# Kernel tuning notes

Measured on AMD Instinct MI355X. Metric: run time of the kernel, lower is better.

## Reference

```python
import jax, jax.numpy as jnp
import numpy as np


def squash(s, axis=-1):
    sq = jnp.sum(jnp.square(s), axis=axis, keepdims=True)
    scale = sq / (1.0 + sq) / (jnp.sqrt(sq) + 1e-08)
    return scale * s


def setup_inputs() -> dict:
    key = jax.random.key(0)
    k1, k2 = jax.random.split(key)
    # [B, input_num_caps, input_dim_caps]
    x = jax.random.normal(k1, (64, 1152, 8), dtype=jnp.float32)
    # W: [input_num_caps, num_capsules, input_dim_caps, dim_capsules]
    W = jax.random.normal(k2, (1152, 32, 8, 16), dtype=jnp.float32) * 0.05
    return {"x": x, "W": W}


def reference(x, W):
    # Original tiles x along the output-capsule axis before the einsum
    # 'bicd,icde->bice'; since the tiled copies are identical along c,
    # this is exactly 'bid,icde->bice' without materializing the tile.
    u_hat = jnp.einsum('bid,icde->bice', x, W)  # [B, I, C, E]
    b = jnp.zeros(u_hat.shape[:3], dtype=u_hat.dtype)  # [B, I, C]
    routings = 3
    v = None
    for i in range(routings):
        c = jax.nn.softmax(b, axis=-1)                 # over output capsules
        s = jnp.einsum('bic,bice->bce', c, u_hat)      # weighted sum over I
        v = squash(s)                                  # [B, C, E]
        if i < routings - 1:
            b = b + jnp.einsum('bice,bce->bic', u_hat, v)  # agreement
    return v
```

## Files before the change

### kernel.cpp

```cpp
#include <hip/hip_runtime.h>
#include <hip/hip_fp16.h>

#define B_ 64
#define I_ 1152
#define C_ 32
#define E_ 16
#define D_ 8
#define BC_ 8
#define ICt 12
#define NIC (I_/ICt)
#define ICX (NIC/8)
#define WROW4 (C_*D_*E_/4)
#define SCE (B_*C_*E_)
#define SCE2 (SCE/2)
#define WIB 8192

__device__ __forceinline__ void gload_lds16(const void* g, void* l) {
  typedef __attribute__((address_space(1))) const void GV;
  typedef __attribute__((address_space(3))) void LV;
  __builtin_amdgcn_global_load_lds((GV*)g, (LV*)l, 16, 0, 0);
}

#define WAITVM8() do { asm volatile("s_waitcnt vmcnt(8)" ::: "memory"); \
                       __builtin_amdgcn_sched_barrier(0); } while (0)
#define WAITVM4() do { asm volatile("s_waitcnt vmcnt(4)" ::: "memory"); \
                       __builtin_amdgcn_sched_barrier(0); } while (0)
#define WAITVM0() do { asm volatile("s_waitcnt vmcnt(0)" ::: "memory"); \
                       __builtin_amdgcn_sched_barrier(0); } while (0)
#define WAITLG0() do { asm volatile("s_waitcnt lgkmcnt(0)" ::: "memory"); \
                       __builtin_amdgcn_sched_barrier(0); } while (0)

typedef _Float16 h2v __attribute__((ext_vector_type(2)));

__device__ __forceinline__ float dot2f(__half2 a, __half2 b, float c) {
#if defined(__has_builtin)
#if __has_builtin(__builtin_amdgcn_fdot2)
  return __builtin_amdgcn_fdot2(__builtin_bit_cast(h2v, a),
                                __builtin_bit_cast(h2v, b), c, false);
#else
  float2 fa = __half22float2(a), fb = __half22float2(b);
  return fmaf(fa.x, fb.x, fmaf(fa.y, fb.y, c));
#endif
#else
  float2 fa = __half22float2(a), fb = __half22float2(b);
  return fmaf(fa.x, fb.x, fmaf(fa.y, fb.y, c));
#endif
}

__device__ __forceinline__ float h2bits(float a, float b) {
  return __builtin_bit_cast(float, __float22half2_rn({a, b}));
}

__global__ __launch_bounds__(256)
void caps_pass0(const float* __restrict__ x, const float* __restrict__ W,
                __half* __restrict__ partial, __half* __restrict__ Wh,
                __half2* __restrict__ xh)
{
  __shared__ float4 Wl[3][1024];
  __shared__ float4 xl[BC_*ICt*2];

  const int t     = threadIdx.x;
  const int c     = t & 31;
  const int eh    = (t >> 5) & 1;
  const int bq    = t >> 6;
  const int xcd   = blockIdx.x & 7;
  const int sl    = blockIdx.x >> 3;
  const int ic    = xcd * ICX + (sl >> 3);
  const int bslab = sl & 7;
  const int b0    = bslab * BC_;
  const int i0    = ic * ICt;

  int fsrc[4];
#pragma unroll
  for (int k = 0; k < 4; ++k) {
    int cc = (t >> 5) + 8*k;
    fsrc[k] = cc*32 + ((c - cc) & 31);
  }

  if (t < BC_*ICt*2) {
    int b = t / (ICt*2), r = t % (ICt*2);
    xl[t] = ((const float4*)x)[ ((size_t)(b0 + b)*I_ + i0)*2 + r ];
  }

  const float4* wg = (const float4*)(W + (size_t)i0 * (C_*D_*E_));
#pragma unroll
  for (int k = 0; k < 4; ++k) gload_lds16(wg + fsrc[k],          &Wl[0][t + 256*k]);
#pragma unroll
  for (int k = 0; k < 4; ++k) gload_lds16(wg + WROW4 + fsrc[k],  &Wl[1][t + 256*k]);

  float acc[2][8];
#pragma unroll
  for (int j = 0; j < 2; ++j)
#pragma unroll
    for (int e = 0; e < 8; ++e) acc[j][e] = 0.f;

  int cur = 0;
  for (int ii = 0; ii < ICt; ++ii) {
    WAITLG0();
    __builtin_amdgcn_s_barrier();
    __builtin_amdgcn_sched_barrier(0);

    if (ii + 2 < ICt) {
      int pre = cur + 2; if (pre >= 3) pre -= 3;
      const float4* wn = wg + (size_t)(ii + 2) * WROW4;
#pragma unroll
      for (int k = 0; k < 4; ++k)
        gload_lds16(wn + fsrc[k], &Wl[pre][t + 256*k]);
    }

    if (ii < ICt - 2)       WAITVM8();
    else if (ii == ICt - 2) WAITVM4();
    else                    WAITVM0();
    __builtin_amdgcn_s_barrier();
    __builtin_amdgcn_sched_barrier(0);

    __builtin_amdgcn_s_setprio(1);
    float xv[2][8];
#pragma unroll
    for (int j = 0; j < 2; ++j) {
      float4 a = xl[(bq*2 + j)*(ICt*2) + ii*2 + 0];
      float4 b = xl[(bq*2 + j)*(ICt*2) + ii*2 + 1];
      xv[j][0]=a.x; xv[j][1]=a.y; xv[j][2]=a.z; xv[j][3]=a.w;
      xv[j][4]=b.x; xv[j][5]=b.y; xv[j][6]=b.z; xv[j][7]=b.w;
    }

    float uh[2][8];
#pragma unroll
    for (int j = 0; j < 2; ++j)
#pragma unroll
      for (int e = 0; e < 8; ++e) uh[j][e] = 0.f;

#pragma unroll
    for (int d = 0; d < D_; ++d) {
#pragma unroll
      for (int qq = 0; qq < 2; ++qq) {
        float4 wv = Wl[cur][c*32 + (((d*4 + eh*2 + qq) + c) & 31)];
        const int eb = qq*4;
#pragma unroll
        for (int j = 0; j < 2; ++j) {
          uh[j][eb+0] = fmaf(xv[j][d], wv.x, uh[j][eb+0]);
          uh[j][eb+1] = fmaf(xv[j][d], wv.y, uh[j][eb+1]);
          uh[j][eb+2] = fmaf(xv[j][d], wv.z, uh[j][eb+2]);
          uh[j][eb+3] = fmaf(xv[j][d], wv.w, uh[j][eb+3]);
        }
      }
    }

#pragma unroll
    for (int j = 0; j < 2; ++j)
#pragma unroll
      for (int e = 0; e < 8; ++e) acc[j][e] = fmaf((1.0f/C_), uh[j][e], acc[j][e]);
    __builtin_amdgcn_s_setprio(0);

    cur = (cur + 1 == 3) ? 0 : cur + 1;
  }

#pragma unroll
  for (int j = 0; j < 2; ++j) {
    size_t base = ((size_t)ic * B_ + (b0 + bq*2 + j)) * (C_*E_) + (size_t)c*E_ + eh*8;
    float4 o;
    o.x = h2bits(acc[j][0], acc[j][1]);
    o.y = h2bits(acc[j][2], acc[j][3]);
    o.z = h2bits(acc[j][4], acc[j][5]);
    o.w = h2bits(acc[j][6], acc[j][7]);
    *(float4*)(partial + base) = o;
  }

  for (int ii = bslab; ii < ICt; ii += 8) {
    const int i = i0 + ii;
    const float4* src = (const float4*)(W + (size_t)i * (C_*D_*E_));
#pragma unroll
    for (int g = 0; g < 2; ++g) {
      int G  = t*2 + g;
      int cc = G >> 4, q = G & 15;
      int d  = q >> 1, eo = q & 1;
      const float4* s4 = src + (cc*8 + d)*4 + eo*2;
      float4 a = s4[0], b = s4[1];
      float4 o;
      o.x = h2bits(a.x, a.y); o.y = h2bits(a.z, a.w);
      o.z = h2bits(b.x, b.y); o.w = h2bits(b.z, b.w);
      *(float4*)(Wh + (size_t)i * 4096 + G*8) = o;
    }
  }
  if (t < BC_*ICt*2) {
    int b = t / (ICt*2), r = t % (ICt*2);
    float4 a = xl[t];
    float4 o;
    o.x = h2bits(a.x, a.x); o.y = h2bits(a.y, a.y);
    o.z = h2bits(a.z, a.z); o.w = h2bits(a.w, a.w);
    size_t idx = ((size_t)(b0 + b)*I_ + (i0 + (r >> 1)))*D_ + (r & 1)*4;
    *(float4*)(xh + idx) = o;
  }
}

template<int MODE>
__global__ __launch_bounds__(256)
void caps_pass_f16(const __half2* __restrict__ xh, const char* __restrict__ Wh,
                   const float* __restrict__ vacc, __half* __restrict__ partial)
{
  __shared__ float4 Wl[3][1024];
  __shared__ __half2 xl[BC_*ICt*D_];

  const int t   = threadIdx.x;
  const int c   = t & 31;
  const int eh  = (t >> 5) & 1;
  const int bq  = t >> 6;
  const int xcd = blockIdx.x & 7;
  const int sl  = blockIdx.x >> 3;
  const int ic  = xcd * ICX + (sl >> 3);
  const int b0  = (sl & 7) * BC_;
  const int i0  = ic * ICt;

  int fsrc[2];
#pragma unroll
  for (int k = 0; k < 2; ++k) {
    int g = t + 256*k, cc = g >> 4, q = g & 15;
    fsrc[k] = cc*256 + ((q ^ (cc & 15)) << 4);
  }

  __half2 vrp[2][4];
#pragma unroll
  for (int j = 0; j < 2; ++j) {
    const float4* vp = (const float4*)(vacc + (((size_t)(b0 + bq*2 + j)*C_ + c)*E_ + eh*8));
    float4 a = vp[0], b = vp[1];
    vrp[j][0] = __float22half2_rn({a.x, a.y});
    vrp[j][1] = __float22half2_rn({a.z, a.w});
    vrp[j][2] = __float22half2_rn({b.x, b.y});
    vrp[j][3] = __float22half2_rn({b.z, b.w});
  }

  if (t < BC_*ICt*D_/4) {
    int b = t / 24, r = t % 24;
    float4 v = ((const float4*)(xh + ((size_t)(b0 + b)*I_ + i0)*D_))[r];
    ((float4*)xl)[b*24 + r] = v;
  }

  const char* wg = Wh + (size_t)i0 * WIB;
#pragma unroll
  for (int k = 0; k < 4; ++k)
    gload_lds16(wg + (k>>1)*WIB + fsrc[k&1], (char*)&Wl[0][0] + (t + 256*k)*16);
#pragma unroll
  for (int k = 0; k < 4; ++k)
    gload_lds16(wg + WIB*2 + (k>>1)*WIB + fsrc[k&1], (char*)&Wl[1][0] + (t + 256*k)*16);

  __half2 accp[2][4];
#pragma unroll
  for (int j = 0; j < 2; ++j)
#pragma unroll
    for (int q = 0; q < 4; ++q) accp[j][q] = __half2{__half(0.f), __half(0.f)};

  int cur = 0;
  for (int p = 0; p < ICt/2; ++p) {
    WAITLG0();
    __builtin_amdgcn_s_barrier();
    __builtin_amdgcn_sched_barrier(0);

    if (p + 2 < ICt/2) {
      int pre = cur + 2; if (pre >= 3) pre -= 3;
      const char* wn = wg + (size_t)(p + 2) * (2*WIB);
#pragma unroll
      for (int k = 0; k < 4; ++k)
        gload_lds16(wn + (k>>1)*WIB + fsrc[k&1], (char*)&Wl[pre][0] + (t + 256*k)*16);
    }

    if (p < ICt/2 - 2)       WAITVM8();
    else if (p == ICt/2 - 2) WAITVM4();
    else                     WAITVM0();
    __builtin_amdgcn_s_barrier();
    __builtin_amdgcn_sched_barrier(0);

    __builtin_amdgcn_s_setprio(1);
#pragma unroll
    for (int il = 0; il < 2; ++il) {
      const int ii = p*2 + il;

      __half2 xd0[8], xd1[8];
      {
        const float4* xr = (const float4*)xl;
        float4 a0 = xr[((bq*2 + 0)*ICt + ii)*2 + 0];
        float4 b0v = xr[((bq*2 + 0)*ICt + ii)*2 + 1];
        float4 a1 = xr[((bq*2 + 1)*ICt + ii)*2 + 0];
        float4 b1v = xr[((bq*2 + 1)*ICt + ii)*2 + 1];
        xd0[0]=__builtin_bit_cast(__half2,a0.x); xd0[1]=__builtin_bit_cast(__half2,a0.y);
        xd0[2]=__builtin_bit_cast(__half2,a0.z); xd0[3]=__builtin_bit_cast(__half2,a0.w);
        xd0[4]=__builtin_bit_cast(__half2,b0v.x); xd0[5]=__builtin_bit_cast(__half2,b0v.y);
        xd0[6]=__builtin_bit_cast(__half2,b0v.z); xd0[7]=__builtin_bit_cast(__half2,b0v.w);
        xd1[0]=__builtin_bit_cast(__half2,a1.x); xd1[1]=__builtin_bit_cast(__half2,a1.y);
        xd1[2]=__builtin_bit_cast(__half2,a1.z); xd1[3]=__builtin_bit_cast(__half2,a1.w);
        xd1[4]=__builtin_bit_cast(__half2,b1v.x); xd1[5]=__builtin_bit_cast(__half2,b1v.y);
        xd1[6]=__builtin_bit_cast(__half2,b1v.z); xd1[7]=__builtin_bit_cast(__half2,b1v.w);
      }

      __half2 uhp[2][4];
#pragma unroll
      for (int j = 0; j < 2; ++j)
#pragma unroll
        for (int q = 0; q < 4; ++q) uhp[j][q] = __half2{__half(0.f), __half(0.f)};

      const char* wrow = (const char*)&Wl[cur][0] + il*WIB + c*256;
#pragma unroll
      for (int d = 0; d < D_; ++d) {
        float4 w4 = *(const float4*)(wrow + ((((d*2 + eh) ^ (c & 15))) << 4));
        __half2 w0 = __builtin_bit_cast(__half2, w4.x);
        __half2 w1 = __builtin_bit_cast(__half2, w4.y);
        __half2 w2 = __builtin_bit_cast(__half2, w4.z);
        __half2 w3 = __builtin_bit_cast(__half2, w4.w);
        uhp[0][0] = __hfma2(xd0[d], w0, uhp[0][0]);
        uhp[0][1] = __hfma2(xd0[d], w1, uhp[0][1]);
        uhp[0][2] = __hfma2(xd0[d], w2, uhp[0][2]);
        uhp[0][3] = __hfma2(xd0[d], w3, uhp[0][3]);
        uhp[1][0] = __hfma2(xd1[d], w0, uhp[1][0]);
        uhp[1][1] = __hfma2(xd1[d], w1, uhp[1][1]);
        uhp[1][2] = __hfma2(xd1[d], w2, uhp[1][2]);
        uhp[1][3] = __hfma2(xd1[d], w3, uhp[1][3]);
      }

      float coef[2];
#pragma unroll
      for (int j = 0; j < 2; ++j) {
        float lg = 0.f;
#pragma unroll
        for (int q = 0; q < 4; ++q) lg = dot2f(uhp[j][q], vrp[j][q], lg);
        lg += __shfl_xor(lg, 32, 64);
        float pexp = __expf(lg);
        float s = pexp;
#pragma unroll
        for (int mk = 16; mk >= 1; mk >>= 1) s += __shfl_xor(s, mk, 64);
        coef[j] = pexp * __builtin_amdgcn_rcpf(s);
      }

#pragma unroll
      for (int j = 0; j < 2; ++j) {
        __half2 cp = __float2half2_rn(coef[j]);
#pragma unroll
        for (int q = 0; q < 4; ++q) accp[j][q] = __hfma2(cp, uhp[j][q], accp[j][q]);
      }
    }
    __builtin_amdgcn_s_setprio(0);

    cur = (cur + 1 == 3) ? 0 : cur + 1;
  }

#pragma unroll
  for (int j = 0; j < 2; ++j) {
    size_t base = ((size_t)ic * B_ + (b0 + bq*2 + j)) * (C_*E_) + (size_t)c*E_ + eh*8;
    float4 o;
    o.x = __builtin_bit_cast(float, accp[j][0]);
    o.y = __builtin_bit_cast(float, accp[j][1]);
    o.z = __builtin_bit_cast(float, accp[j][2]);
    o.w = __builtin_bit_cast(float, accp[j][3]);
    *(float4*)(partial + base) = o;
  }
}

__global__ __launch_bounds__(256)
void reduce_squash(const __half2* __restrict__ partial, float* __restrict__ vacc,
                   float* __restrict__ out, int mode)
{
  __shared__ float2 sm[256];
  const int t    = threadIdx.x;
  const int pair = blockIdx.x*32 + (t & 31);
  const int part = t >> 5;
  const __half2* p = partial + (size_t)(part*(NIC/8)) * SCE2 + pair;
  float2 s = {0.f, 0.f};
#pragma unroll
  for (int k = 0; k < NIC/8; ++k) {
    float2 f = __half22float2(p[(size_t)k * SCE2]);
    s.x += f.x; s.y += f.y;
  }
  sm[t] = s;
  __syncthreads();
  if (t < 32) {
    float2 tot = {0.f, 0.f};
#pragma unroll
    for (int pp = 0; pp < 8; ++pp) {
      float2 v = sm[t + 32*pp];
      tot.x += v.x; tot.y += v.y;
    }
    float sq = tot.x*tot.x + tot.y*tot.y;
    sq += __shfl_xor(sq, 1); sq += __shfl_xor(sq, 2); sq += __shfl_xor(sq, 4);
    float scale = sq / (1.f + sq) / (sqrtf(sq) + 1e-8f);
    float vx = scale * tot.x, vy = scale * tot.y;
    const int cell = pair * 2;
    if (mode == 0)      { vacc[cell] = vx;  vacc[cell+1] = vy;  }
    else if (mode == 1) { vacc[cell] += vx; vacc[cell+1] += vy; }
    else                { out[cell]  = vx;  out[cell+1]  = vy;  }
  }
}

extern "C" void kernel_launch(void* const* d_in, const int* in_sizes, int n_in,
                              void* d_out, int out_size, void* d_ws, size_t ws_size,
                              hipStream_t stream)
{
  const float* x = (const float*)d_in[0];
  const float* W = (const float*)d_in[1];
  float* out     = (float*)d_out;

  char* ws = (char*)d_ws;
  __half*  partial = (__half*)ws;                    ws += (size_t)NIC*SCE*2;
  float*   vacc    = (float*)ws;                     ws += (size_t)SCE*4;
  __half*  Wh      = (__half*)ws;                    ws += (size_t)I_*C_*D_*E_*2;
  __half2* xh      = (__half2*)ws;

  dim3 pg(NIC * (B_/BC_));
  const int rg = SCE2 / 32;

  caps_pass0<<<pg, 256, 0, stream>>>(x, W, partial, Wh, xh);
  reduce_squash<<<rg, 256, 0, stream>>>((const __half2*)partial, vacc, nullptr, 0);
  caps_pass_f16<0><<<pg, 256, 0, stream>>>(xh, (const char*)Wh, vacc, partial);
  reduce_squash<<<rg, 256, 0, stream>>>((const __half2*)partial, vacc, nullptr, 1);
  caps_pass_f16<1><<<pg, 256, 0, stream>>>(xh, (const char*)Wh, vacc, partial);
  reduce_squash<<<rg, 256, 0, stream>>>((const __half2*)partial, vacc, out, 2);
}
```

Measured before the change: 65.96 us.

## Halve batch tile per block in f16 routing passes, doubling grid size

The f16 routing-pass kernel now gives each block 4 batch rows instead of 8, with one row per thread quarter. The per-iteration weight stage holds one input capsule instead of two, and the pipeline wait counts are adjusted to match. The aim is more blocks and less LDS per block, for better occupancy and latency hiding. The cost is that each W tile is streamed from global or L2 twice as often across blocks, and there is less register-level reuse of each loaded weight.

```diff
diff --git a/kernel.cpp b/kernel.cpp
--- a/kernel.cpp
+++ b/kernel.cpp
@@ -25,6 +25,8 @@
                        __builtin_amdgcn_sched_barrier(0); } while (0)
 #define WAITVM4() do { asm volatile("s_waitcnt vmcnt(4)" ::: "memory"); \
                        __builtin_amdgcn_sched_barrier(0); } while (0)
+#define WAITVM2() do { asm volatile("s_waitcnt vmcnt(2)" ::: "memory"); \
+                       __builtin_amdgcn_sched_barrier(0); } while (0)
 #define WAITVM0() do { asm volatile("s_waitcnt vmcnt(0)" ::: "memory"); \
                        __builtin_amdgcn_sched_barrier(0); } while (0)
 #define WAITLG0() do { asm volatile("s_waitcnt lgkmcnt(0)" ::: "memory"); \
@@ -198,8 +200,8 @@
 void caps_pass_f16(const __half2* __restrict__ xh, const char* __restrict__ Wh,
                    const float* __restrict__ vacc, __half* __restrict__ partial)
 {
-  __shared__ float4 Wl[3][1024];
-  __shared__ __half2 xl[BC_*ICt*D_];
+  __shared__ float4 Wl[3][512];
+  __shared__ __half2 xl[4*ICt*D_];
 
   const int t   = threadIdx.x;
   const int c   = t & 31;
@@ -207,8 +209,8 @@
   const int bq  = t >> 6;
   const int xcd = blockIdx.x & 7;
   const int sl  = blockIdx.x >> 3;
-  const int ic  = xcd * ICX + (sl >> 3);
-  const int b0  = (sl & 7) * BC_;
+  const int ic  = xcd * ICX + (sl >> 4);
+  const int b0  = (sl & 15) * 4;
   const int i0  = ic * ICt;
 
   int fsrc[2];
@@ -218,18 +220,17 @@
     fsrc[k] = cc*256 + ((q ^ (cc & 15)) << 4);
   }
 
-  __half2 vrp[2][4];
-#pragma unroll
-  for (int j = 0; j < 2; ++j) {
-    const float4* vp = (const float4*)(vacc + (((size_t)(b0 + bq*2 + j)*C_ + c)*E_ + eh*8));
+  __half2 vrp[4];
+  {
+    const float4* vp = (const float4*)(vacc + (((size_t)(b0 + bq)*C_ + c)*E_ + eh*8));
     float4 a = vp[0], b = vp[1];
-    vrp[j][0] = __float22half2_rn({a.x, a.y});
-    vrp[j][1] = __float22half2_rn({a.z, a.w});
-    vrp[j][2] = __float22half2_rn({b.x, b.y});
-    vrp[j][3] = __float22half2_rn({b.z, b.w});
-  }
-
-  if (t < BC_*ICt*D_/4) {
+    vrp[0] = __float22half2_rn({a.x, a.y});
+    vrp[1] = __float22half2_rn({a.z, a.w});
+    vrp[2] = __float22half2_rn({b.x, b.y});
+    vrp[3] = __float22half2_rn({b.z, b.w});
+  }
+
+  if (t < 4*ICt*D_/4) {
     int b = t / 24, r = t % 24;
     float4 v = ((const float4*)(xh + ((size_t)(b0 + b)*I_ + i0)*D_))[r];
     ((float4*)xl)[b*24 + r] = v;
@@ -237,118 +238,85 @@
 
   const char* wg = Wh + (size_t)i0 * WIB;
 #pragma unroll
-  for (int k = 0; k < 4; ++k)
-    gload_lds16(wg + (k>>1)*WIB + fsrc[k&1], (char*)&Wl[0][0] + (t + 256*k)*16);
-#pragma unroll
-  for (int k = 0; k < 4; ++k)
-    gload_lds16(wg + WIB*2 + (k>>1)*WIB + fsrc[k&1], (char*)&Wl[1][0] + (t + 256*k)*16);
-
-  __half2 accp[2][4];
-#pragma unroll
-  for (int j = 0; j < 2; ++j)
-#pragma unroll
-    for (int q = 0; q < 4; ++q) accp[j][q] = __half2{__half(0.f), __half(0.f)};
+  for (int k = 0; k < 2; ++k) gload_lds16(wg + fsrc[k],       (char*)&Wl[0][0] + (t + 256*k)*16);
+#pragma unroll
+  for (int k = 0; k < 2; ++k) gload_lds16(wg + WIB + fsrc[k], (char*)&Wl[1][0] + (t + 256*k)*16);
+
+  __half2 accp[4];
+#pragma unroll
+  for (int q = 0; q < 4; ++q) accp[q] = __half2{__half(0.f), __half(0.f)};
 
   int cur = 0;
-  for (int p = 0; p < ICt/2; ++p) {
+  for (int ii = 0; ii < ICt; ++ii) {
     WAITLG0();
     __builtin_amdgcn_s_barrier();
     __builtin_amdgcn_sched_barrier(0);
 
-    if (p + 2 < ICt/2) {
+    if (ii + 2 < ICt) {
       int pre = cur + 2; if (pre >= 3) pre -= 3;
-      const char* wn = wg + (size_t)(p + 2) * (2*WIB);
-#pragma unroll
-      for (int k = 0; k < 4; ++k)
-        gload_lds16(wn + (k>>1)*WIB + fsrc[k&1], (char*)&Wl[pre][0] + (t + 256*k)*16);
-    }
-
-    if (p < ICt/2 - 2)       WAITVM8();
-    else if (p == ICt/2 - 2) WAITVM4();
-    else                     WAITVM0();
+      const char* wn = wg + (size_t)(ii + 2) * WIB;
+#pragma unroll
+      for (int k = 0; k < 2; ++k)
+        gload_lds16(wn + fsrc[k], (char*)&Wl[pre][0] + (t + 256*k)*16);
+    }
+
+    if (ii < ICt - 2)       WAITVM4();
+    else if (ii == ICt - 2) WAITVM2();
+    else                    WAITVM0();
     __builtin_amdgcn_s_barrier();
     __builtin_amdgcn_sched_barrier(0);
 
     __builtin_amdgcn_s_setprio(1);
-#pragma unroll
-    for (int il = 0; il < 2; ++il) {
-      const int ii = p*2 + il;
-
-      __half2 xd0[8], xd1[8];
-      {
-        const float4* xr = (const float4*)xl;
-        float4 a0 = xr[((bq*2 + 0)*ICt + ii)*2 + 0];
-        float4 b0v = xr[((bq*2 + 0)*ICt + ii)*2 + 1];
-        float4 a1 = xr[((bq*2 + 1)*ICt + ii)*2 + 0];
-        float4 b1v = xr[((bq*2 + 1)*ICt + ii)*2 + 1];
-        xd0[0]=__builtin_bit_cast(__half2,a0.x); xd0[1]=__builtin_bit_cast(__half2,a0.y);
-        xd0[2]=__builtin_bit_cast(__half2,a0.z); xd0[3]=__builtin_bit_cast(__half2,a0.w);
-        xd0[4]=__builtin_bit_cast(__half2,b0v.x); xd0[5]=__builtin_bit_cast(__half2,b0v.y);
-        xd0[6]=__builtin_bit_cast(__half2,b0v.z); xd0[7]=__builtin_bit_cast(__half2,b0v.w);
-        xd1[0]=__builtin_bit_cast(__half2,a1.x); xd1[1]=__builtin_bit_cast(__half2,a1.y);
-        xd1[2]=__builtin_bit_cast(__half2,a1.z); xd1[3]=__builtin_bit_cast(__half2,a1.w);
-        xd1[4]=__builtin_bit_cast(__half2,b1v.x); xd1[5]=__builtin_bit_cast(__half2,b1v.y);
-        xd1[6]=__builtin_bit_cast(__half2,b1v.z); xd1[7]=__builtin_bit_cast(__half2,b1v.w);
-      }
-
-      __half2 uhp[2][4];
-#pragma unroll
-      for (int j = 0; j < 2; ++j)
-#pragma unroll
-        for (int q = 0; q < 4; ++q) uhp[j][q] = __half2{__half(0.f), __half(0.f)};
-
-      const char* wrow = (const char*)&Wl[cur][0] + il*WIB + c*256;
-#pragma unroll
-      for (int d = 0; d < D_; ++d) {
-        float4 w4 = *(const float4*)(wrow + ((((d*2 + eh) ^ (c & 15))) << 4));
-        __half2 w0 = __builtin_bit_cast(__half2, w4.x);
-        __half2 w1 = __builtin_bit_cast(__half2, w4.y);
-        __half2 w2 = __builtin_bit_cast(__half2, w4.z);
-        __half2 w3 = __builtin_bit_cast(__half2, w4.w);
-        uhp[0][0] = __hfma2(xd0[d], w0, uhp[0][0]);
-        uhp[0][1] = __hfma2(xd0[d], w1, uhp[0][1]);
-        uhp[0][2] = __hfma2(xd0[d], w2, uhp[0][2]);
-        uhp[0][3] = __hfma2(xd0[d], w3, uhp[0][3]);
-        uhp[1][0] = __hfma2(xd1[d], w0, uhp[1][0]);
-        uhp[1][1] = __hfma2(xd1[d], w1, uhp[1][1]);
-        uhp[1][2] = __hfma2(xd1[d], w2, uhp[1][2]);
-        uhp[1][3] = __hfma2(xd1[d], w3, uhp[1][3]);
-      }
-
-      float coef[2];
-#pragma unroll
-      for (int j = 0; j < 2; ++j) {
-        float lg = 0.f;
-#pragma unroll
-        for (int q = 0; q < 4; ++q) lg = dot2f(uhp[j][q], vrp[j][q], lg);
-        lg += __shfl_xor(lg, 32, 64);
-        float pexp = __expf(lg);
-        float s = pexp;
-#pragma unroll
-        for (int mk = 16; mk >= 1; mk >>= 1) s += __shfl_xor(s, mk, 64);
-        coef[j] = pexp * __builtin_amdgcn_rcpf(s);
-      }
-
-#pragma unroll
-      for (int j = 0; j < 2; ++j) {
-        __half2 cp = __float2half2_rn(coef[j]);
-#pragma unroll
-        for (int q = 0; q < 4; ++q) accp[j][q] = __hfma2(cp, uhp[j][q], accp[j][q]);
-      }
-    }
+    __half2 xd[8];
+    {
+      const float4* xr = (const float4*)xl;
+      float4 a = xr[(bq*ICt + ii)*2 + 0];
+      float4 b = xr[(bq*ICt + ii)*2 + 1];
+      xd[0]=__builtin_bit_cast(__half2,a.x); xd[1]=__builtin_bit_cast(__half2,a.y);
+      xd[2]=__builtin_bit_cast(__half2,a.z); xd[3]=__builtin_bit_cast(__half2,a.w);
+      xd[4]=__builtin_bit_cast(__half2,b.x); xd[5]=__builtin_bit_cast(__half2,b.y);
+      xd[6]=__builtin_bit_cast(__half2,b.z); xd[7]=__builtin_bit_cast(__half2,b.w);
+    }
+
+    __half2 uhp[4];
+#pragma unroll
+    for (int q = 0; q < 4; ++q) uhp[q] = __half2{__half(0.f), __half(0.f)};
+
+    const char* wrow = (const char*)&Wl[cur][0] + c*256;
+#pragma unroll
+    for (int d = 0; d < D_; ++d) {
+      float4 w4 = *(const float4*)(wrow + ((((d*2 + eh) ^ (c & 15))) << 4));
+      uhp[0] = __hfma2(xd[d], __builtin_bit_cast(__half2, w4.x), uhp[0]);
+      uhp[1] = __hfma2(xd[d], __builtin_bit_cast(__half2, w4.y), uhp[1]);
+      uhp[2] = __hfma2(xd[d], __builtin_bit_cast(__half2, w4.z), uhp[2]);
+      uhp[3] = __hfma2(xd[d], __builtin_bit_cast(__half2, w4.w), uhp[3]);
+    }
+
+    float lg = 0.f;
+#pragma unroll
+    for (int q = 0; q < 4; ++q) lg = dot2f(uhp[q], vrp[q], lg);
+    lg += __shfl_xor(lg, 32, 64);
+    float pexp = __expf(lg);
+    float s = pexp;
+#pragma unroll
+    for (int mk = 16; mk >= 1; mk >>= 1) s += __shfl_xor(s, mk, 64);
+    float coef = pexp * __builtin_amdgcn_rcpf(s);
+
+    __half2 cp = __float2half2_rn(coef);
+#pragma unroll
+    for (int q = 0; q < 4; ++q) accp[q] = __hfma2(cp, uhp[q], accp[q]);
     __builtin_amdgcn_s_setprio(0);
 
     cur = (cur + 1 == 3) ? 0 : cur + 1;
   }
 
-#pragma unroll
-  for (int j = 0; j < 2; ++j) {
-    size_t base = ((size_t)ic * B_ + (b0 + bq*2 + j)) * (C_*E_) + (size_t)c*E_ + eh*8;
+  {
+    size_t base = ((size_t)ic * B_ + (b0 + bq)) * (C_*E_) + (size_t)c*E_ + eh*8;
     float4 o;
-    o.x = __builtin_bit_cast(float, accp[j][0]);
-    o.y = __builtin_bit_cast(float, accp[j][1]);
-    o.z = __builtin_bit_cast(float, accp[j][2]);
-    o.w = __builtin_bit_cast(float, accp[j][3]);
+    o.x = __builtin_bit_cast(float, accp[0]);
+    o.y = __builtin_bit_cast(float, accp[1]);
+    o.z = __builtin_bit_cast(float, accp[2]);
+    o.w = __builtin_bit_cast(float, accp[3]);
     *(float4*)(partial + base) = o;
   }
 }
@@ -402,13 +370,14 @@
   __half*  Wh      = (__half*)ws;                    ws += (size_t)I_*C_*D_*E_*2;
   __half2* xh      = (__half2*)ws;
 
-  dim3 pg(NIC * (B_/BC_));
+  dim3 p0(NIC * (B_/BC_));
+  dim3 pf(NIC * (B_/4));
   const int rg = SCE2 / 32;
 
-  caps_pass0<<<pg, 256, 0, stream>>>(x, W, partial, Wh, xh);
+  caps_pass0<<<p0, 256, 0, stream>>>(x, W, partial, Wh, xh);
   reduce_squash<<<rg, 256, 0, stream>>>((const __half2*)partial, vacc, nullptr, 0);
-  caps_pass_f16<0><<<pg, 256, 0, stream>>>(xh, (const char*)Wh, vacc, partial);
+  caps_pass_f16<1><<<pf, 256, 0, stream>>>(xh, (const char*)Wh, vacc, partial);
   reduce_squash<<<rg, 256, 0, stream>>>((const __half2*)partial, vacc, nullptr, 1);
-  caps_pass_f16<1><<<pg, 256, 0, stream>>>(xh, (const char*)Wh, vacc, partial);
+  caps_pass_f16<2><<<pf, 256, 0, stream>>>(xh, (const char*)Wh, vacc, partial);
   reduce_squash<<<rg, 256, 0, stream>>>((const __half2*)partial, vacc, out, 2);
 }
```

Result: slower. 72.57 us (+10.0%).
